# Kernel tuning notes

Measured on AMD Instinct MI355X. Metric: run time of the kernel, lower is better.

Reference implementation:

```python
import jax, jax.numpy as jnp
import numpy as np

DIM = 1024
NUM_HEADS = 16
HEAD_DIM = DIM // NUM_HEADS


def setup_inputs() -> dict:
    key = jax.random.key(0)
    k1, k2, k3, k4, k5, k6 = jax.random.split(key, 6)
    B, T, C = 4, 2048, DIM
    s = 1.0 / np.sqrt(C)
    return {
        "x": jax.random.normal(k1, (B, T, C), dtype=jnp.float32),
        "attn_bias": jax.random.normal(k2, (B, T, T), dtype=jnp.float32),
        "qkv_w": jax.random.uniform(k3, (3 * C, C), dtype=jnp.float32, minval=-s, maxval=s),
        "qkv_b": jax.random.uniform(k4, (3 * C,), dtype=jnp.float32, minval=-s, maxval=s),
        "out_w": jax.random.uniform(k5, (C, C), dtype=jnp.float32, minval=-s, maxval=s),
        "out_b": jax.random.uniform(k6, (C,), dtype=jnp.float32, minval=-s, maxval=s),
    }


def reference(x, attn_bias, qkv_w, qkv_b, out_w, out_b):
    B, T, C = x.shape
    H, D = NUM_HEADS, HEAD_DIM
    # fused QKV projection (torch Linear: x @ W^T + b)
    qkv = jnp.einsum('btc,fc->btf', x, qkv_w) + qkv_b  # [B,T,3C]
    q, k, v = jnp.split(qkv, 3, axis=-1)
    q = q.reshape(B, T, H, D).transpose(0, 2, 1, 3)  # [B,H,T,D]
    k = k.reshape(B, T, H, D).transpose(0, 2, 1, 3)
    v = v.reshape(B, T, H, D).transpose(0, 2, 1, 3)
    scores = jnp.einsum('bhtd,bhsd->bhts', q, k) / jnp.sqrt(jnp.float32(D))
    scores = scores + attn_bias[:, None, :, :]  # 3-D bias -> broadcast over heads
    attn = jax.nn.softmax(scores, axis=-1)
    out = jnp.einsum('bhts,bhsd->bhtd', attn, v)  # [B,H,T,D]
    out = out.transpose(0, 2, 1, 3).reshape(B, T, C)
    return jnp.einsum('btc,fc->btf', out, out_w) + out_b
```

## Files before the change

### kernel.cpp

```cpp
#include <hip/hip_runtime.h>

#define BATCH 4
#define SEQ   2048
#define CDIM  1024
#define HEADS 16
#define HDIM  64
#define N3    3072
#define NTOK  8192
#define QKP   2048
#define LOG2E 1.44269504f
#define QSC   0.18033688f

typedef __attribute__((ext_vector_type(4))) float    float4v;
typedef __attribute__((ext_vector_type(8))) short    short8;
typedef __attribute__((ext_vector_type(8))) __bf16   bf16x8;
typedef __attribute__((ext_vector_type(4))) _Float16 half4v;
typedef __attribute__((ext_vector_type(8))) _Float16 half8v;
typedef __attribute__((ext_vector_type(2))) _Float16 half2v;

__device__ __forceinline__ unsigned short f2bf(float f) {
    union { float f; unsigned int u; } x; x.f = f;
    unsigned int r = x.u + 0x7fffu + ((x.u >> 16) & 1u);
    return (unsigned short)(r >> 16);
}

__device__ __forceinline__ bf16x8 ld_bf8(const unsigned short* p) {
    short8 s = *(const short8*)p;
    return __builtin_bit_cast(bf16x8, s);
}

__device__ __forceinline__ void glds16(const void* g, void* l) {
    __builtin_amdgcn_global_load_lds(
        (const __attribute__((address_space(1))) void*)g,
        (__attribute__((address_space(3))) void*)l, 16, 0, 0);
}

__global__ void cast3_f32_bf16(const float* __restrict__ a, int na4,
                               const float* __restrict__ b, int nb4,
                               const float* __restrict__ c, int nc4,
                               unsigned short* __restrict__ oa,
                               unsigned short* __restrict__ ob,
                               unsigned short* __restrict__ oc) {
    int i = blockIdx.x * blockDim.x + threadIdx.x;
    const float* src; unsigned short* dst; int j = i;
    if (j < na4)            { src = a; dst = oa; }
    else if ((j -= na4) < nb4) { src = b; dst = ob; }
    else if ((j -= nb4) < nc4) { src = c; dst = oc; }
    else return;
    float4v v = ((const float4v*)src)[j];
    ushort4 r;
    r.x = f2bf(v[0]); r.y = f2bf(v[1]); r.z = f2bf(v[2]); r.w = f2bf(v[3]);
    ((ushort4*)dst)[j] = r;
}

__global__ __launch_bounds__(256, 3)
void gemm_bt(const unsigned short* __restrict__ A,
             const unsigned short* __restrict__ Bm,
             const float* __restrict__ bias,
             void* __restrict__ Cout,
             void* __restrict__ Cout2,
             int M, int N, int K, int mode)
{
    __shared__ alignas(16) unsigned short SMEM[2 * 128 * 64];
    unsigned short* As = SMEM;
    unsigned short* Bs = SMEM + 128 * 64;

    const int tid  = threadIdx.x;
    const int lane = tid & 63;
    const int wave = tid >> 6;
    const int wr = wave >> 1, wc = wave & 1;
    const int lm = lane & 15, quad = lane >> 4;

    const int nwg  = gridDim.x * gridDim.y;
    const int d    = blockIdx.y * gridDim.x + blockIdx.x;
    const int orig = (d & 7) * (nwg >> 3) + (d >> 3);
    const int bix  = orig % gridDim.x;
    const int biy  = orig / gridDim.x;

    const size_t m0 = (size_t)biy * 128;
    const size_t n0 = (size_t)bix * 128;

    const unsigned short* ag[4];
    const unsigned short* bg[4];
    unsigned short* la[4];
    unsigned short* lb[4];
#pragma unroll
    for (int i = 0; i < 4; i++) {
        int idx = tid + i * 256;
        int row = idx >> 3;
        int lc  = (idx & 7) ^ (row & 7);
        ag[i] = &A [(m0 + row) * K + lc * 8];
        bg[i] = &Bm[(n0 + row) * K + lc * 8];
        la[i] = &As[(idx & ~63) * 8];
        lb[i] = &Bs[(idx & ~63) * 8];
    }

    float4v acc[4][4];
#pragma unroll
    for (int i = 0; i < 4; i++)
#pragma unroll
        for (int j = 0; j < 4; j++) acc[i][j] = (float4v){0.f, 0.f, 0.f, 0.f};

    for (int k0 = 0; k0 < K; k0 += 64) {
#pragma unroll
        for (int i = 0; i < 4; i++) glds16(ag[i], la[i]);
#pragma unroll
        for (int i = 0; i < 4; i++) glds16(bg[i], lb[i]);
#pragma unroll
        for (int i = 0; i < 4; i++) { ag[i] += 64; bg[i] += 64; }
        __syncthreads();
#pragma unroll
        for (int kk = 0; kk < 2; kk++) {
            bf16x8 af[4], bfr[4];
#pragma unroll
            for (int t = 0; t < 4; t++) {
                int slot = ((quad + kk * 4) ^ (lm & 7)) * 8;
                af [t] = ld_bf8(&As[(wr * 64 + t * 16 + lm) * 64 + slot]);
                bfr[t] = ld_bf8(&Bs[(wc * 64 + t * 16 + lm) * 64 + slot]);
            }
#pragma unroll
            for (int ti = 0; ti < 4; ti++)
#pragma unroll
                for (int tj = 0; tj < 4; tj++)
                    acc[ti][tj] = __builtin_amdgcn_mfma_f32_16x16x32_bf16(
                        af[ti], bfr[tj], acc[ti][tj], 0, 0, 0);
        }
        __syncthreads();
    }

    const bool vpath = (mode == 1) && ((int)n0 >= 2 * CDIM);

    if (!vpath) {
#pragma unroll
        for (int ti = 0; ti < 4; ti++) {
            size_t row = m0 + wr * 64 + ti * 16 + quad * 4;
#pragma unroll
            for (int tj = 0; tj < 4; tj++) {
                int col = (int)n0 + wc * 64 + tj * 16 + lm;
                float bv = bias[col];
                if (mode == 0) {
#pragma unroll
                    for (int r = 0; r < 4; r++)
                        ((float*)Cout)[(row + r) * N + col] = acc[ti][tj][r] + bv;
                } else {
                    float scl = (col < CDIM) ? QSC : 1.0f;
#pragma unroll
                    for (int r = 0; r < 4; r++)
                        ((unsigned short*)Cout)[(row + r) * QKP + col] =
                            f2bf((acc[ti][tj][r] + bv) * scl);
                }
            }
        }
    } else {
        half4v hv[4][4];
#pragma unroll
        for (int ti = 0; ti < 4; ti++)
#pragma unroll
            for (int tj = 0; tj < 4; tj++) {
                int col = (int)n0 + wc * 64 + tj * 16 + lm;
                float bv = bias[col];
#pragma unroll
                for (int r = 0; r < 4; r++)
                    hv[ti][tj][r] = (_Float16)(acc[ti][tj][r] + bv);
            }

        const int bbv = (int)(m0 >> 11);
        const int s0  = (int)(m0 & 2047);
        unsigned short* LT = SMEM;

#pragma unroll
        for (int p = 0; p < 2; ++p) {
            __syncthreads();
            if (wc == p) {
#pragma unroll
                for (int ti = 0; ti < 4; ti++) {
                    int ssb = wr * 64 + ti * 16 + quad * 4;
                    int p16 = (ssb >> 3);
                    int w8  = (ssb >> 2) & 1;
#pragma unroll
                    for (int tj = 0; tj < 4; tj++) {
                        int dd = tj * 16 + lm;
                        *(half4v*)&LT[dd * 136 + ((p16 ^ (dd & 15)) * 8) + w8 * 4] =
                            hv[ti][tj];
                    }
                }
            }
            __syncthreads();
#pragma unroll
            for (int i = 0; i < 4; ++i) {
                int dd   = i * 16 + (tid >> 4);
                int u16  = tid & 15;
                int win  = u16 >> 3, u = u16 & 7;
                int base = (u < 4) ? u : (u + 4);
                int ssa  = win * 64 + base * 4;
                int ssb2 = ssa + 16;
                half4v va = *(const half4v*)&LT[dd * 136 +
                    (((ssa >> 3) ^ (dd & 15)) * 8) + ((ssa >> 2) & 1) * 4];
                half4v vb = *(const half4v*)&LT[dd * 136 +
                    (((ssb2 >> 3) ^ (dd & 15)) * 8) + ((ssb2 >> 2) & 1) * 4];
                half8v vv;
                vv[0] = va[0]; vv[1] = va[1]; vv[2] = va[2]; vv[3] = va[3];
                vv[4] = vb[0]; vv[5] = vb[1]; vv[6] = vb[2]; vv[7] = vb[3];
                size_t gr = (size_t)bbv * CDIM + ((int)n0 - 2 * CDIM) + p * 64 + dd;
                *(half8v*)((unsigned short*)Cout2 + gr * SEQ + s0 + u16 * 8) = vv;
            }
        }
    }
}

__global__ __launch_bounds__(256, 4)
void attn_kernel(const unsigned short* __restrict__ qk,
                 const unsigned short* __restrict__ vT,
                 const float* __restrict__ bias,
                 unsigned short* __restrict__ outp)
{
    __shared__ alignas(16) char smem[32768];
    float*          BiasS = (float*)smem;
    unsigned short* Qs    = (unsigned short*)smem;
    unsigned short* Ks    = (unsigned short*)(smem + 16384);
    unsigned short* Vts   = (unsigned short*)(smem + 24576);

    const int tid  = threadIdx.x;
    const int lane = tid & 63, wave = tid >> 6;
    const int lm = lane & 15, quad = lane >> 4;
    const int q0 = blockIdx.x * 64;
    const int bh = blockIdx.y;
    const int bb = bh >> 4, h = bh & 15;
    const size_t rowbase = (size_t)bb * SEQ;
    const unsigned short* vTh = vT + (size_t)bh * HDIM * SEQ;
    const float* biasb = bias + (size_t)bb * SEQ * SEQ + (size_t)q0 * SEQ;

#pragma unroll
    for (int i = 0; i < 2; i++) {
        int idx = tid + i * 256;
        int row = idx >> 3;
        int lc  = (idx & 7) ^ (row & 7);
        glds16(&qk[(rowbase + q0 + row) * QKP + h * 64 + lc * 8], &Qs[(idx & ~63) * 8]);
    }
    __syncthreads();
    bf16x8 bq[2];
#pragma unroll
    for (int kk = 0; kk < 2; kk++)
        bq[kk] = ld_bf8(&Qs[(wave * 16 + lm) * 64 + (((quad + kk * 4) ^ (lm & 7)) * 8)]);

    const unsigned short *kg0, *kg1, *vg0, *vg1;
    unsigned short *lk0, *lk1, *lv0, *lv1;
    {
        int idx = tid, row = idx >> 3, lc = (idx & 7) ^ (row & 7);
        kg0 = &qk[(rowbase + row) * QKP + CDIM + h * 64 + lc * 8];
        vg0 = &vTh[(size_t)row * SEQ + lc * 8];
        lk0 = &Ks[(idx & ~63) * 8];
        lv0 = &Vts[(idx & ~63) * 8];
        idx = tid + 256; row = idx >> 3; lc = (idx & 7) ^ (row & 7);
        kg1 = &qk[(rowbase + row) * QKP + CDIM + h * 64 + lc * 8];
        vg1 = &vTh[(size_t)row * SEQ + lc * 8];
        lk1 = &Ks[(idx & ~63) * 8];
        lv1 = &Vts[(idx & ~63) * 8];
    }
    const float* bgp[4];
    float*       lbp[4];
#pragma unroll
    for (int i = 0; i < 4; i++) {
        int idx = tid + i * 256;
        int row = idx >> 4;
        int lc  = (idx & 15) ^ (row & 15);
        bgp[i] = &biasb[(size_t)row * SEQ + lc * 4];
        lbp[i] = &BiasS[(idx & ~63) * 4];
    }

    const half8v vones8 = {(_Float16)1.f, (_Float16)1.f, (_Float16)1.f, (_Float16)1.f,
                           (_Float16)1.f, (_Float16)1.f, (_Float16)1.f, (_Float16)1.f};
    float4v rs4 = (float4v){0.f, 0.f, 0.f, 0.f};
    float4v o[4];
#pragma unroll
    for (int t = 0; t < 4; t++) o[t] = (float4v){0.f, 0.f, 0.f, 0.f};

    for (int it = 0; it < SEQ / 64; ++it) {
        __syncthreads();
        glds16(kg0, lk0); glds16(kg1, lk1);
        glds16(vg0, lv0); glds16(vg1, lv1);
#pragma unroll
        for (int i = 0; i < 4; i++) glds16(bgp[i], lbp[i]);
        kg0 += 64 * QKP; kg1 += 64 * QKP;
        vg0 += 64; vg1 += 64;
#pragma unroll
        for (int i = 0; i < 4; i++) bgp[i] += 64;
        __syncthreads();

        float4v st[4];
#pragma unroll
        for (int tj = 0; tj < 4; ++tj) {
            float4v bv = *(const float4v*)&BiasS[(wave * 16 + lm) * 64 +
                                                 (((tj * 4 + quad) ^ lm) * 4)];
            st[tj] = bv * LOG2E;
            bf16x8 ak0 = ld_bf8(&Ks[(tj * 16 + lm) * 64 + (((quad    ) ^ (lm & 7)) * 8)]);
            bf16x8 ak1 = ld_bf8(&Ks[(tj * 16 + lm) * 64 + (((quad + 4) ^ (lm & 7)) * 8)]);
            st[tj] = __builtin_amdgcn_mfma_f32_16x16x32_bf16(ak0, bq[0], st[tj], 0, 0, 0);
            st[tj] = __builtin_amdgcn_mfma_f32_16x16x32_bf16(ak1, bq[1], st[tj], 0, 0, 0);
        }

        half8v pq[2];
#pragma unroll
        for (int tj = 0; tj < 4; ++tj) {
            float p0 = __builtin_amdgcn_exp2f(st[tj][0]);
            float p1 = __builtin_amdgcn_exp2f(st[tj][1]);
            float p2 = __builtin_amdgcn_exp2f(st[tj][2]);
            float p3 = __builtin_amdgcn_exp2f(st[tj][3]);
            half2v plo = __builtin_bit_cast(half2v, __builtin_amdgcn_cvt_pkrtz(p0, p1));
            half2v phi = __builtin_bit_cast(half2v, __builtin_amdgcn_cvt_pkrtz(p2, p3));
            pq[tj >> 1][(tj & 1) * 4 + 0] = plo[0];
            pq[tj >> 1][(tj & 1) * 4 + 1] = plo[1];
            pq[tj >> 1][(tj & 1) * 4 + 2] = phi[0];
            pq[tj >> 1][(tj & 1) * 4 + 3] = phi[1];
        }

        rs4 = __builtin_amdgcn_mfma_f32_16x16x32_f16(pq[0], vones8, rs4, 0, 0, 0);
        rs4 = __builtin_amdgcn_mfma_f32_16x16x32_f16(pq[1], vones8, rs4, 0, 0, 0);

        __builtin_amdgcn_s_setprio(1);
#pragma unroll
        for (int tjp = 0; tjp < 2; ++tjp) {
#pragma unroll
            for (int dt = 0; dt < 4; ++dt) {
                int row = dt * 16 + lm;
                half8v v8 = *(const half8v*)&Vts[row * 64 +
                               (((tjp * 4 + quad) ^ (lm & 7)) * 8)];
                o[dt] = __builtin_amdgcn_mfma_f32_16x16x32_f16(pq[tjp], v8, o[dt], 0, 0, 0);
            }
        }
        __builtin_amdgcn_s_setprio(0);
    }

    float i4[4];
#pragma unroll
    for (int r = 0; r < 4; r++) i4[r] = 1.0f / rs4[r];
#pragma unroll
    for (int dt = 0; dt < 4; dt++) {
        int col = h * 64 + dt * 16 + lm;
#pragma unroll
        for (int r = 0; r < 4; r++) {
            size_t trow = rowbase + q0 + wave * 16 + quad * 4 + r;
            outp[trow * CDIM + col] = f2bf(o[dt][r] * i4[r]);
        }
    }
}

extern "C" void kernel_launch(void* const* d_in, const int* in_sizes, int n_in,
                              void* d_out, int out_size, void* d_ws, size_t ws_size,
                              hipStream_t stream)
{
    const float* x         = (const float*)d_in[0];
    const float* attn_bias = (const float*)d_in[1];
    const float* qkv_w     = (const float*)d_in[2];
    const float* qkv_b     = (const float*)d_in[3];
    const float* out_w     = (const float*)d_in[4];
    const float* out_b     = (const float*)d_in[5];
    float* out = (float*)d_out;

    char* p = (char*)d_ws;
    unsigned short* x_bf   = (unsigned short*)p; p += (size_t)NTOK * CDIM * 2;
    unsigned short* wq_bf  = (unsigned short*)p; p += (size_t)N3 * CDIM * 2;
    unsigned short* wo_bf  = (unsigned short*)p; p += (size_t)CDIM * CDIM * 2;
    unsigned short* qk_bf  = (unsigned short*)p; p += (size_t)NTOK * QKP * 2;
    unsigned short* vT_f16 = (unsigned short*)p; p += (size_t)BATCH * CDIM * SEQ * 2;
    unsigned short* at_bf  = (unsigned short*)p;

    const int na4 = NTOK * CDIM / 4;
    const int nb4 = N3 * CDIM / 4;
    const int nc4 = CDIM * CDIM / 4;
    const int nt4 = na4 + nb4 + nc4;
    cast3_f32_bf16<<<(nt4 + 255) / 256, 256, 0, stream>>>(
        x, na4, qkv_w, nb4, out_w, nc4, x_bf, wq_bf, wo_bf);

    gemm_bt<<<dim3(N3 / 128, NTOK / 128), 256, 0, stream>>>(
        x_bf, wq_bf, qkv_b, qk_bf, vT_f16, NTOK, N3, CDIM, 1);

    attn_kernel<<<dim3(SEQ / 64, BATCH * HEADS), 256, 0, stream>>>(
        qk_bf, vT_f16, attn_bias, at_bf);

    gemm_bt<<<dim3(CDIM / 128, NTOK / 128), 256, 0, stream>>>(
        at_bf, wo_bf, out_b, out, nullptr, NTOK, CDIM, CDIM, 0);
}
```

Baseline: 348.6 us.

## Process two heads per attention block to share bias tile loads

The attention kernel now computes two adjacent heads per block. It loads the fp32 attention bias tile once per key tile and reuses it for both heads, roughly halving the dominant bias read traffic. The block index is also remapped so blocks sharing a batch and query range land on the same XCD, for better L2 reuse. In exchange, shared memory grows to 48KB, occupancy drops to 3 blocks per CU, and the grid halves to 1024 blocks, with more accumulator registers per thread.

```diff
diff --git a/kernel.cpp b/kernel.cpp
--- a/kernel.cpp
+++ b/kernel.cpp
@@ -208,57 +208,75 @@
     }
 }
 
-__global__ __launch_bounds__(256, 4)
+__global__ __launch_bounds__(256, 3)
 void attn_kernel(const unsigned short* __restrict__ qk,
                  const unsigned short* __restrict__ vT,
                  const float* __restrict__ bias,
                  unsigned short* __restrict__ outp)
 {
-    __shared__ alignas(16) char smem[32768];
+    __shared__ alignas(16) char smem[49152];
     float*          BiasS = (float*)smem;
-    unsigned short* Qs    = (unsigned short*)smem;
+    unsigned short* QsP   = (unsigned short*)smem;
     unsigned short* Ks    = (unsigned short*)(smem + 16384);
-    unsigned short* Vts   = (unsigned short*)(smem + 24576);
+    unsigned short* Vts0  = (unsigned short*)(smem + 32768);
+    unsigned short* Vts1  = (unsigned short*)(smem + 40960);
 
     const int tid  = threadIdx.x;
     const int lane = tid & 63, wave = tid >> 6;
     const int lm = lane & 15, quad = lane >> 4;
-    const int q0 = blockIdx.x * 64;
-    const int bh = blockIdx.y;
-    const int bb = bh >> 4, h = bh & 15;
+
+    const int d   = blockIdx.y * 32 + blockIdx.x;
+    const int xcd = d & 7;
+    const int j   = d >> 3;
+    const int hp  = j & 7;
+    const int g   = xcd * 16 + (j >> 3);
+    const int bb  = g >> 5;
+    const int q0  = (g & 31) * 64;
+    const int h0  = hp * 2;
+
     const size_t rowbase = (size_t)bb * SEQ;
-    const unsigned short* vTh = vT + (size_t)bh * HDIM * SEQ;
+    const unsigned short* vTh0 = vT + (size_t)(bb * 16 + h0) * HDIM * SEQ;
+    const unsigned short* vTh1 = vTh0 + (size_t)HDIM * SEQ;
     const float* biasb = bias + (size_t)bb * SEQ * SEQ + (size_t)q0 * SEQ;
 
+#pragma unroll
+    for (int i = 0; i < 4; i++) {
+        int idx = tid + i * 256;
+        int row = idx >> 4;
+        int lc  = (idx & 15) ^ (row & 15);
+        glds16(&qk[(rowbase + q0 + row) * QKP + h0 * 64 + lc * 8],
+               &QsP[(idx & ~63) * 8]);
+    }
+    __syncthreads();
+    bf16x8 bq[2][2];
+#pragma unroll
+    for (int hh = 0; hh < 2; ++hh)
+#pragma unroll
+        for (int kk = 0; kk < 2; ++kk)
+            bq[hh][kk] = ld_bf8(&QsP[(wave * 16 + lm) * 128 +
+                                     (((hh * 8 + quad + kk * 4) ^ lm) * 8)]);
+
+    const unsigned short* kgp[4];  unsigned short* lkp[4];
+#pragma unroll
+    for (int i = 0; i < 4; i++) {
+        int idx = tid + i * 256;
+        int row = idx >> 4;
+        int lc  = (idx & 15) ^ (row & 15);
+        kgp[i] = &qk[(rowbase + row) * QKP + CDIM + h0 * 64 + lc * 8];
+        lkp[i] = &Ks[(idx & ~63) * 8];
+    }
+    const unsigned short *vg0[2], *vg1[2];  unsigned short *lv0[2], *lv1[2];
 #pragma unroll
     for (int i = 0; i < 2; i++) {
         int idx = tid + i * 256;
         int row = idx >> 3;
         int lc  = (idx & 7) ^ (row & 7);
-        glds16(&qk[(rowbase + q0 + row) * QKP + h * 64 + lc * 8], &Qs[(idx & ~63) * 8]);
-    }
-    __syncthreads();
-    bf16x8 bq[2];
-#pragma unroll
-    for (int kk = 0; kk < 2; kk++)
-        bq[kk] = ld_bf8(&Qs[(wave * 16 + lm) * 64 + (((quad + kk * 4) ^ (lm & 7)) * 8)]);
-
-    const unsigned short *kg0, *kg1, *vg0, *vg1;
-    unsigned short *lk0, *lk1, *lv0, *lv1;
-    {
-        int idx = tid, row = idx >> 3, lc = (idx & 7) ^ (row & 7);
-        kg0 = &qk[(rowbase + row) * QKP + CDIM + h * 64 + lc * 8];
-        vg0 = &vTh[(size_t)row * SEQ + lc * 8];
-        lk0 = &Ks[(idx & ~63) * 8];
-        lv0 = &Vts[(idx & ~63) * 8];
-        idx = tid + 256; row = idx >> 3; lc = (idx & 7) ^ (row & 7);
-        kg1 = &qk[(rowbase + row) * QKP + CDIM + h * 64 + lc * 8];
-        vg1 = &vTh[(size_t)row * SEQ + lc * 8];
-        lk1 = &Ks[(idx & ~63) * 8];
-        lv1 = &Vts[(idx & ~63) * 8];
-    }
-    const float* bgp[4];
-    float*       lbp[4];
+        vg0[i] = &vTh0[(size_t)row * SEQ + lc * 8];
+        vg1[i] = &vTh1[(size_t)row * SEQ + lc * 8];
+        lv0[i] = &Vts0[(idx & ~63) * 8];
+        lv1[i] = &Vts1[(idx & ~63) * 8];
+    }
+    const float* bgp[4];  float* lbp[4];
 #pragma unroll
     for (int i = 0; i < 4; i++) {
         int idx = tid + i * 256;
@@ -270,77 +288,95 @@
 
     const half8v vones8 = {(_Float16)1.f, (_Float16)1.f, (_Float16)1.f, (_Float16)1.f,
                            (_Float16)1.f, (_Float16)1.f, (_Float16)1.f, (_Float16)1.f};
-    float4v rs4 = (float4v){0.f, 0.f, 0.f, 0.f};
-    float4v o[4];
-#pragma unroll
-    for (int t = 0; t < 4; t++) o[t] = (float4v){0.f, 0.f, 0.f, 0.f};
+    float4v rs[2];
+    rs[0] = (float4v){0.f, 0.f, 0.f, 0.f};
+    rs[1] = (float4v){0.f, 0.f, 0.f, 0.f};
+    float4v o[2][4];
+#pragma unroll
+    for (int hh = 0; hh < 2; ++hh)
+#pragma unroll
+        for (int t = 0; t < 4; t++) o[hh][t] = (float4v){0.f, 0.f, 0.f, 0.f};
 
     for (int it = 0; it < SEQ / 64; ++it) {
         __syncthreads();
-        glds16(kg0, lk0); glds16(kg1, lk1);
-        glds16(vg0, lv0); glds16(vg1, lv1);
+#pragma unroll
+        for (int i = 0; i < 4; i++) glds16(kgp[i], lkp[i]);
+        glds16(vg0[0], lv0[0]); glds16(vg0[1], lv0[1]);
+        glds16(vg1[0], lv1[0]); glds16(vg1[1], lv1[1]);
 #pragma unroll
         for (int i = 0; i < 4; i++) glds16(bgp[i], lbp[i]);
-        kg0 += 64 * QKP; kg1 += 64 * QKP;
-        vg0 += 64; vg1 += 64;
-#pragma unroll
-        for (int i = 0; i < 4; i++) bgp[i] += 64;
+#pragma unroll
+        for (int i = 0; i < 4; i++) { kgp[i] += 64 * QKP; bgp[i] += 64; }
+#pragma unroll
+        for (int i = 0; i < 2; i++) {
+            vg0[i] += 64; vg1[i] += 64;
+        }
         __syncthreads();
 
-        float4v st[4];
-#pragma unroll
-        for (int tj = 0; tj < 4; ++tj) {
-            float4v bv = *(const float4v*)&BiasS[(wave * 16 + lm) * 64 +
-                                                 (((tj * 4 + quad) ^ lm) * 4)];
-            st[tj] = bv * LOG2E;
-            bf16x8 ak0 = ld_bf8(&Ks[(tj * 16 + lm) * 64 + (((quad    ) ^ (lm & 7)) * 8)]);
-            bf16x8 ak1 = ld_bf8(&Ks[(tj * 16 + lm) * 64 + (((quad + 4) ^ (lm & 7)) * 8)]);
-            st[tj] = __builtin_amdgcn_mfma_f32_16x16x32_bf16(ak0, bq[0], st[tj], 0, 0, 0);
-            st[tj] = __builtin_amdgcn_mfma_f32_16x16x32_bf16(ak1, bq[1], st[tj], 0, 0, 0);
-        }
-
-        half8v pq[2];
-#pragma unroll
-        for (int tj = 0; tj < 4; ++tj) {
-            float p0 = __builtin_amdgcn_exp2f(st[tj][0]);
-            float p1 = __builtin_amdgcn_exp2f(st[tj][1]);
-            float p2 = __builtin_amdgcn_exp2f(st[tj][2]);
-            float p3 = __builtin_amdgcn_exp2f(st[tj][3]);
-            half2v plo = __builtin_bit_cast(half2v, __builtin_amdgcn_cvt_pkrtz(p0, p1));
-            half2v phi = __builtin_bit_cast(half2v, __builtin_amdgcn_cvt_pkrtz(p2, p3));
-            pq[tj >> 1][(tj & 1) * 4 + 0] = plo[0];
-            pq[tj >> 1][(tj & 1) * 4 + 1] = plo[1];
-            pq[tj >> 1][(tj & 1) * 4 + 2] = phi[0];
-            pq[tj >> 1][(tj & 1) * 4 + 3] = phi[1];
-        }
-
-        rs4 = __builtin_amdgcn_mfma_f32_16x16x32_f16(pq[0], vones8, rs4, 0, 0, 0);
-        rs4 = __builtin_amdgcn_mfma_f32_16x16x32_f16(pq[1], vones8, rs4, 0, 0, 0);
-
-        __builtin_amdgcn_s_setprio(1);
-#pragma unroll
-        for (int tjp = 0; tjp < 2; ++tjp) {
-#pragma unroll
-            for (int dt = 0; dt < 4; ++dt) {
-                int row = dt * 16 + lm;
-                half8v v8 = *(const half8v*)&Vts[row * 64 +
-                               (((tjp * 4 + quad) ^ (lm & 7)) * 8)];
-                o[dt] = __builtin_amdgcn_mfma_f32_16x16x32_f16(pq[tjp], v8, o[dt], 0, 0, 0);
-            }
-        }
-        __builtin_amdgcn_s_setprio(0);
-    }
-
-    float i4[4];
-#pragma unroll
-    for (int r = 0; r < 4; r++) i4[r] = 1.0f / rs4[r];
-#pragma unroll
-    for (int dt = 0; dt < 4; dt++) {
-        int col = h * 64 + dt * 16 + lm;
-#pragma unroll
-        for (int r = 0; r < 4; r++) {
-            size_t trow = rowbase + q0 + wave * 16 + quad * 4 + r;
-            outp[trow * CDIM + col] = f2bf(o[dt][r] * i4[r]);
+#pragma unroll
+        for (int hh = 0; hh < 2; ++hh) {
+            const unsigned short* Vt = hh ? Vts1 : Vts0;
+
+            float4v st[4];
+#pragma unroll
+            for (int tj = 0; tj < 4; ++tj) {
+                float4v bv = *(const float4v*)&BiasS[(wave * 16 + lm) * 64 +
+                                                     (((tj * 4 + quad) ^ lm) * 4)];
+                st[tj] = bv * LOG2E;
+                bf16x8 ak0 = ld_bf8(&Ks[(tj * 16 + lm) * 128 +
+                                        (((hh * 8 + quad    ) ^ lm) * 8)]);
+                bf16x8 ak1 = ld_bf8(&Ks[(tj * 16 + lm) * 128 +
+                                        (((hh * 8 + quad + 4) ^ lm) * 8)]);
+                st[tj] = __builtin_amdgcn_mfma_f32_16x16x32_bf16(ak0, bq[hh][0], st[tj], 0, 0, 0);
+                st[tj] = __builtin_amdgcn_mfma_f32_16x16x32_bf16(ak1, bq[hh][1], st[tj], 0, 0, 0);
+            }
+
+            half8v pq[2];
+#pragma unroll
+            for (int tj = 0; tj < 4; ++tj) {
+                float p0 = __builtin_amdgcn_exp2f(st[tj][0]);
+                float p1 = __builtin_amdgcn_exp2f(st[tj][1]);
+                float p2 = __builtin_amdgcn_exp2f(st[tj][2]);
+                float p3 = __builtin_amdgcn_exp2f(st[tj][3]);
+                half2v plo = __builtin_bit_cast(half2v, __builtin_amdgcn_cvt_pkrtz(p0, p1));
+                half2v phi = __builtin_bit_cast(half2v, __builtin_amdgcn_cvt_pkrtz(p2, p3));
+                pq[tj >> 1][(tj & 1) * 4 + 0] = plo[0];
+                pq[tj >> 1][(tj & 1) * 4 + 1] = plo[1];
+                pq[tj >> 1][(tj & 1) * 4 + 2] = phi[0];
+                pq[tj >> 1][(tj & 1) * 4 + 3] = phi[1];
+            }
+
+            rs[hh] = __builtin_amdgcn_mfma_f32_16x16x32_f16(pq[0], vones8, rs[hh], 0, 0, 0);
+            rs[hh] = __builtin_amdgcn_mfma_f32_16x16x32_f16(pq[1], vones8, rs[hh], 0, 0, 0);
+
+            __builtin_amdgcn_s_setprio(1);
+#pragma unroll
+            for (int tjp = 0; tjp < 2; ++tjp) {
+#pragma unroll
+                for (int dt = 0; dt < 4; ++dt) {
+                    int row = dt * 16 + lm;
+                    half8v v8 = *(const half8v*)&Vt[row * 64 +
+                                   (((tjp * 4 + quad) ^ (lm & 7)) * 8)];
+                    o[hh][dt] = __builtin_amdgcn_mfma_f32_16x16x32_f16(pq[tjp], v8, o[hh][dt], 0, 0, 0);
+                }
+            }
+            __builtin_amdgcn_s_setprio(0);
+        }
+    }
+
+#pragma unroll
+    for (int hh = 0; hh < 2; ++hh) {
+        float i4[4];
+#pragma unroll
+        for (int r = 0; r < 4; r++) i4[r] = 1.0f / rs[hh][r];
+#pragma unroll
+        for (int dt = 0; dt < 4; dt++) {
+            int col = (h0 + hh) * 64 + dt * 16 + lm;
+#pragma unroll
+            for (int r = 0; r < 4; r++) {
+                size_t trow = rowbase + q0 + wave * 16 + quad * 4 + r;
+                outp[trow * CDIM + col] = f2bf(o[hh][dt][r] * i4[r]);
+            }
         }
     }
 }
@@ -375,7 +411,7 @@
     gemm_bt<<<dim3(N3 / 128, NTOK / 128), 256, 0, stream>>>(
         x_bf, wq_bf, qkv_b, qk_bf, vT_f16, NTOK, N3, CDIM, 1);
 
-    attn_kernel<<<dim3(SEQ / 64, BATCH * HEADS), 256, 0, stream>>>(
+    attn_kernel<<<dim3(32, 32), 256, 0, stream>>>(
         qk_bf, vT_f16, attn_bias, at_bf);
 
     gemm_bt<<<dim3(CDIM / 128, NTOK / 128), 256, 0, stream>>>(
```

Measured after the change: 345.7 us. No clear change (-0.8%).
